# Optimization experiments

Hardware: AMD Instinct MI355X
Metric: run time of the kernel (lower is better)

## Reference

```python
import jax, jax.numpy as jnp
import numpy as np

T_STEPS = 128
N_RAYS = 16384
RAY_EXT = 10.0  # ray_ext_factor


def _posenc(x, n_freq=4):
    # x: (...,3) in [-1,1] -> (...,3 + 3*2*n_freq) = (...,27)
    feats = [x]
    for k in range(n_freq):
        f = (2.0 ** k) * jnp.pi
        feats.append(jnp.sin(f * x))
        feats.append(jnp.cos(f * x))
    return jnp.concatenate(feats, -1)


def _sh_deg2(d):
    # real spherical harmonics, degree 0 and 1 (4 coeffs), d unit vectors (...,3)
    x, y, z = d[..., 0], d[..., 1], d[..., 2]
    c0 = 0.28209479177387814
    c1 = 0.4886025119029199
    return jnp.stack([jnp.full_like(x, c0), c1 * y, c1 * z, c1 * x], -1)


def _forward(rays_o, rays_d, tnoise, aabb, W1, b1, W2, b2, Wc1, bc1, Wc2, bc2):
    # --- ray-AABB intersection (slab method), RayBundle.intersect_aabb ---
    inv_d = 1.0 / rays_d
    t0 = (aabb[0] - rays_o) * inv_d
    t1 = (aabb[1] - rays_o) * inv_d
    tnear = jnp.maximum(jnp.max(jnp.minimum(t0, t1), -1, keepdims=True), 0.0)  # (N,1)
    tfar = jnp.min(jnp.maximum(t0, t1), -1, keepdims=True)                      # (N,1)
    active = (tfar > tnear).astype(rays_o.dtype)  # active_mask; masking replaces compaction

    # --- StratifiedRayStepSampler: ts (T,N,1) ---
    T = tnoise.shape[0]
    base = (jnp.arange(T, dtype=rays_o.dtype)[:, None, None] + tnoise) / T
    ts = tnear[None] + (tfar - tnear)[None] * base
    xyz = rays_o[None] + ts * rays_d[None]  # (T,N,3)

    # --- vol.sample(xyz, ynm, return_color=True): density + color MLP ---
    xn = 2.0 * (xyz - aabb[0]) / (aabb[1] - aabb[0]) - 1.0
    enc = _posenc(xn)                             # (T,N,27)
    h = jax.nn.relu(enc @ W1 + b1)                # (T,N,64)
    dh = h @ W2 + b2                              # (T,N,16)
    sigma = jnp.exp(dh[..., :1])                  # (T,N,1) density
    feat = dh[..., 1:]                            # (T,N,15)
    dnorm = jnp.linalg.norm(rays_d, axis=-1, keepdims=True)  # (N,1)
    ynm = _sh_deg2(rays_d / dnorm)                # encode_raydir -> (N,4)
    ynm = jnp.broadcast_to(ynm[None], (T,) + ynm.shape)      # expand to (T,N,4)
    hc = jax.nn.relu(jnp.concatenate([feat, ynm], -1) @ Wc1 + bc1)
    rgb = jax.nn.sigmoid(hc @ Wc2 + bc2)          # (T,N,3)

    # --- integrate_timesteps: transmittance-weighted compositing ---
    tfinal = tfar * RAY_EXT
    delta = jnp.concatenate([ts[1:] - ts[:-1], tfinal[None] - ts[-1:]], 0)  # (T,N,1)
    sd = sigma * delta * dnorm[None]
    alpha = 1.0 - jnp.exp(-sd)
    trans = jnp.exp(-(jnp.cumsum(sd, 0) - sd))    # exclusive cumsum transmittance
    w = trans * alpha * active[None]              # (T,N,1); inactive rays -> zero maps

    color = jnp.sum(w * rgb, 0)                   # color_map  (N,3)
    alpha_map = jnp.sum(w, 0)                     # alpha_map  (N,1)
    return jnp.concatenate([color, alpha_map], -1)  # rgba (N,4)


def setup_inputs() -> dict:
    key = jax.random.key(0)
    ks = jax.random.split(key, 8)
    # origins on a sphere of radius 2.5 around the unit aabb, aimed at points inside it
    o = jax.random.normal(ks[0], (N_RAYS, 3), jnp.float32)
    o = 2.5 * o / jnp.linalg.norm(o, axis=-1, keepdims=True)
    tgt = jax.random.uniform(ks[1], (N_RAYS, 3), jnp.float32, -0.5, 0.5)
    d = tgt - o
    d = d / jnp.linalg.norm(d, axis=-1, keepdims=True)
    aabb = jnp.array([[-1.0, -1.0, -1.0], [1.0, 1.0, 1.0]], jnp.float32)
    tnoise = jax.random.uniform(ks[2], (T_STEPS, N_RAYS, 1), jnp.float32)
    s1, s2, s3, s4 = 27 ** -0.5, 64 ** -0.5, 19 ** -0.5, 64 ** -0.5
    return {
        'rays_o': o, 'rays_d': d, 'tnoise': tnoise, 'aabb': aabb,
        'W1': jax.random.normal(ks[3], (27, 64), jnp.float32) * s1,
        'b1': jnp.zeros((64,), jnp.float32),
        'W2': jax.random.normal(ks[4], (64, 16), jnp.float32) * (0.1 * s2),
        'b2': jnp.zeros((16,), jnp.float32),
        'Wc1': jax.random.normal(ks[5], (19, 64), jnp.float32) * s3,
        'bc1': jnp.zeros((64,), jnp.float32),
        'Wc2': jax.random.normal(ks[6], (64, 3), jnp.float32) * s4,
        'bc2': jnp.zeros((3,), jnp.float32),
    }


def reference(rays_o, rays_d, tnoise, aabb, W1, b1, W2, b2, Wc1, bc1, Wc2, bc2):
    return _forward(rays_o, rays_d, tnoise, aabb, W1, b1, W2, b2, Wc1, bc1, Wc2, bc2)
```

## Files before the change

kernel.cpp:

```cpp
#include <hip/hip_runtime.h>
#include <stdint.h>

#define N_RAYS  16384
#define T_STEPS 128
#define RPW   16
#define WAVES 4
#define TSEG  32

typedef _Float16 half8  __attribute__((ext_vector_type(8)));
typedef _Float16 half4  __attribute__((ext_vector_type(4)));
typedef __fp16   fp16x2 __attribute__((ext_vector_type(2)));
typedef float    float4_ __attribute__((ext_vector_type(4)));
typedef uint32_t uint2_  __attribute__((ext_vector_type(2)));

#define H8_W1    0
#define H8_W2    256
#define H8_WC2   384
#define H_WC1K16 4096
#define F32_CV   3072
#define F32_BC2  3392
#define F32_S0   3408

__device__ __forceinline__ uint32_t pk(float a, float b) {
    fp16x2 h = __builtin_amdgcn_cvt_pkrtz(a, b);
    return __builtin_bit_cast(uint32_t, h);
}
__device__ __forceinline__ uint32_t pkr(float a, float b) {
    fp16x2 h = __builtin_amdgcn_cvt_pkrtz(a, b);
    fp16x2 z = {(__fp16)0.f, (__fp16)0.f};
    fp16x2 m = __builtin_elementwise_max(h, z);
    return __builtin_bit_cast(uint32_t, m);
}

__global__ void prep_weights(const float* __restrict__ W1, const float* __restrict__ b1,
                             const float* __restrict__ W2, const float* __restrict__ b2,
                             const float* __restrict__ Wc1, const float* __restrict__ bc1,
                             const float* __restrict__ Wc2, const float* __restrict__ bc2,
                             void* __restrict__ ws) {
    _Float16* wh = (_Float16*)ws;
    float*    wf = (float*)ws;
    int frag = blockIdx.x;
    int lane = threadIdx.x;
    int mm = lane & 15, q = lane >> 4;
    if (frag < 4) {
        int tau = frag;
        int n = tau * 16 + mm;
        for (int j = 0; j < 8; ++j) {
            float w;
            if (j < 6)      w = W1[(3 + 6 * q + j) * 64 + n];
            else if (j == 6) w = (q == 0) ? W1[0 * 64 + n] : (q == 1) ? W1[2 * 64 + n] : 0.f;
            else             w = (q == 0) ? W1[1 * 64 + n] : (q == 1) ? b1[n] : 0.f;
            wh[(H8_W1 + tau * 64 + lane) * 8 + j] = (_Float16)w;
        }
    } else if (frag < 6) {
        int kap = frag - 4;
        for (int j = 0; j < 8; ++j) {
            int k = kap * 32 + q * 8 + j;
            wh[(H8_W2 + kap * 64 + lane) * 8 + j] = (_Float16)W2[k * 16 + mm];
        }
    } else if (frag < 10) {
        int tau = frag - 6;
        int n2 = tau * 16 + mm;
        for (int j = 0; j < 4; ++j) {
            int k = 4 * q + j;
            float w = (k == 0) ? 0.f : Wc1[(k - 1) * 64 + n2];
            wh[H_WC1K16 + (tau * 64 + lane) * 4 + j] = (_Float16)w;
        }
    } else if (frag < 12) {
        int kap = frag - 10;
        for (int j = 0; j < 8; ++j) {
            int k = kap * 32 + q * 8 + j;
            wh[(H8_WC2 + kap * 64 + lane) * 8 + j] =
                (_Float16)((mm < 3) ? Wc2[k * 3 + mm] : 0.f);
        }
    } else {
        int n = lane;
        wf[F32_CV + 0 * 64 + n] = Wc1[15 * 64 + n];
        wf[F32_CV + 1 * 64 + n] = Wc1[16 * 64 + n];
        wf[F32_CV + 2 * 64 + n] = Wc1[17 * 64 + n];
        wf[F32_CV + 3 * 64 + n] = Wc1[18 * 64 + n];
        float cc = bc1[n];
        for (int c = 0; c < 15; ++c) cc += b2[1 + c] * Wc1[c * 64 + n];
        wf[F32_CV + 4 * 64 + n] = cc;
        if (lane < 16) wf[F32_BC2 + lane] = (lane < 3) ? bc2[lane] : 0.f;
        if (lane == 0) wf[F32_S0] = b2[0];
    }
}

__global__ __launch_bounds__(256, 4)
void render_kernel(const float* __restrict__ rays_o, const float* __restrict__ rays_d,
                   const float* __restrict__ tnoise, const float* __restrict__ aabb,
                   const void* __restrict__ ws, float* __restrict__ out) {
    __shared__ __align__(16) _Float16 sH[WAVES][2][1024];
    __shared__ float sComb[WAVES][RPW][5];

    const int tid  = threadIdx.x;
    const int wv   = tid >> 6;
    const int lane = tid & 63;
    const int m    = lane & 15;
    const int q    = lane >> 4;
    const int r    = blockIdx.x * RPW + m;

    const half8* wsv  = (const half8*)ws;
    const half4* wsv4 = (const half4*)((const _Float16*)ws + H_WC1K16);
    const float* wsf  = (const float*)ws;
    half8 fW1[4], fW2[2], fWc2[2];
    half4 fWc1[4];
    #pragma unroll
    for (int i = 0; i < 4; ++i) fW1[i]  = wsv[H8_W1  + i * 64 + lane];
    #pragma unroll
    for (int i = 0; i < 2; ++i) fW2[i]  = wsv[H8_W2  + i * 64 + lane];
    #pragma unroll
    for (int i = 0; i < 2; ++i) fWc2[i] = wsv[H8_WC2 + i * 64 + lane];
    #pragma unroll
    for (int i = 0; i < 4; ++i) fWc1[i] = wsv4[i * 64 + lane];
    const float4_ binit = ((const float4_*)(wsf + F32_BC2))[q];
    const float s0b = wsf[F32_S0];

    float o0 = rays_o[r * 3 + 0], o1 = rays_o[r * 3 + 1], o2 = rays_o[r * 3 + 2];
    float d0 = rays_d[r * 3 + 0], d1 = rays_d[r * 3 + 1], d2 = rays_d[r * 3 + 2];
    float a00 = aabb[0], a01 = aabb[1], a02 = aabb[2];
    float a10 = aabb[3], a11 = aabb[4], a12 = aabb[5];

    float i0 = 1.0f / d0, i1 = 1.0f / d1, i2 = 1.0f / d2;
    float u0 = (a00 - o0) * i0, v0 = (a10 - o0) * i0;
    float u1 = (a01 - o1) * i1, v1 = (a11 - o1) * i1;
    float u2 = (a02 - o2) * i2, v2 = (a12 - o2) * i2;
    float tnear = fmaxf(fmaxf(fmaxf(fminf(u0, v0), fminf(u1, v1)), fminf(u2, v2)), 0.0f);
    float tfar  = fminf(fminf(fmaxf(u0, v0), fmaxf(u1, v1)), fmaxf(u2, v2));
    bool active = (tfar > tnear);
    float dt = tfar - tnear;
    float dt128 = dt * (1.0f / 128.0f);

    float dn  = sqrtf(d0 * d0 + d1 * d1 + d2 * d2);
    float idn = 1.0f / dn;
    const float c0sh = 0.28209479177387814f;
    const float c1sh = 0.4886025119029199f;
    float y1 = c1sh * d1 * idn, y2 = c1sh * d2 * idn, y3 = c1sh * d0 * idn;

    float4_ cv[4];
    #pragma unroll
    for (int tau = 0; tau < 4; ++tau) {
        #pragma unroll
        for (int reg = 0; reg < 4; ++reg) {
            int n = tau * 16 + 4 * q + reg;
            float c = wsf[F32_CV + 4 * 64 + n];
            c = fmaf(c0sh, wsf[F32_CV + 0 * 64 + n], c);
            c = fmaf(y1,   wsf[F32_CV + 1 * 64 + n], c);
            c = fmaf(y2,   wsf[F32_CV + 2 * 64 + n], c);
            c = fmaf(y3,   wsf[F32_CV + 3 * 64 + n], c);
            cv[tau][reg] = c;
        }
    }

    float qs = 0.5f * (float)(1 << q);
    float sc0 = 2.0f / (a10 - a00), of0 = -a00 * sc0 - 1.0f;
    float sc1 = 2.0f / (a11 - a01), of1 = -a01 * sc1 - 1.0f;
    float sc2 = 2.0f / (a12 - a02), of2 = -a02 * sc2 - 1.0f;
    float scq0 = sc0 * qs, ofq0 = of0 * qs;
    float scq1 = sc1 * qs, ofq1 = of1 * qs;
    float scq2 = sc2 * qs, ofq2 = of2 * qs;

    _Float16*       hwp[2];
    const _Float16* hrp[2];
    #pragma unroll
    for (int p = 0; p < 2; ++p) {
        hwp[p] = &sH[wv][p][((q >> 1) * 16 + m) * 8 + 4 * (q & 1)];
        hrp[p] = &sH[wv][p][(q * 16 + m) * 8];
    }

    const float4_ z4 = {0.f, 0.f, 0.f, 0.f};
    const bool q0 = (q == 0), q1 = (q == 1);

    float trans = 1.0f, sdtot = 0.0f, wacc = 0.0f;
    float cacc0 = 0.0f, cacc1 = 0.0f, cacc2 = 0.0f;

    const int tbase = wv * TSEG;
    float nA = tnoise[(tbase + 0) * N_RAYS + r];
    float nB = tnoise[(tbase + 1) * N_RAYS + r];

    #pragma unroll 1
    for (int tt = 0; tt < TSEG; tt += 2) {
        const int t0 = tbase + tt, t1 = t0 + 1;
        float nC = (t0 + 2 < T_STEPS) ? tnoise[(t0 + 2) * N_RAYS + r] : 0.0f;
        float nD = (t0 + 3 < T_STEPS) ? tnoise[(t0 + 3) * N_RAYS + r] : 0.0f;
        float ts0 = fmaf((float)t0 + nA, dt128, tnear);
        float ts1 = fmaf((float)t1 + nB, dt128, tnear);
        float ts2 = fmaf((float)(t0 + 2) + nC, dt128, tnear);
        float tsP[2] = {ts0, ts1};
        float deltaP[2];
        deltaP[0] = ts1 - ts0;
        deltaP[1] = (t1 < T_STEPS - 1) ? (ts2 - ts1) : fmaf(tfar, 10.0f, -ts1);
        nA = nC; nB = nD;

        float dhx[2];
        float4_ rgbP[2];

        #pragma unroll
        for (int p = 0; p < 2; ++p) {
            float x = fmaf(tsP[p], d0, o0);
            float y = fmaf(tsP[p], d1, o1);
            float z = fmaf(tsP[p], d2, o2);
            float xr0 = fmaf(x, scq0, ofq0);
            float xr1 = fmaf(y, scq1, ofq1);
            float xr2 = fmaf(z, scq2, ofq2);
            float s0 = __builtin_amdgcn_sinf(xr0);
            float s1 = __builtin_amdgcn_sinf(xr1);
            float s2 = __builtin_amdgcn_sinf(xr2);
            float cA = __builtin_amdgcn_cosf(xr0);
            float cB = __builtin_amdgcn_cosf(xr1);
            float cC = __builtin_amdgcn_cosf(xr2);
            float e6 = q0 ? (xr0 + xr0) : (q1 ? xr2 : 0.0f);
            float e7 = q0 ? (xr1 + xr1) : (q1 ? 1.0f : 0.0f);
            union { uint32_t u[4]; half8 h; } xf_;
            xf_.u[0] = pk(s0, s1); xf_.u[1] = pk(s2, cA);
            xf_.u[2] = pk(cB, cC); xf_.u[3] = pk(e6, e7);
            half8 xf = xf_.h;

            float4_ h0 = __builtin_amdgcn_mfma_f32_16x16x32_f16(fW1[0], xf, z4, 0, 0, 0);
            float4_ h1 = __builtin_amdgcn_mfma_f32_16x16x32_f16(fW1[1], xf, z4, 0, 0, 0);
            float4_ h2 = __builtin_amdgcn_mfma_f32_16x16x32_f16(fW1[2], xf, z4, 0, 0, 0);
            float4_ h3 = __builtin_amdgcn_mfma_f32_16x16x32_f16(fW1[3], xf, z4, 0, 0, 0);
            uint2_ w;
            w.x = pkr(h0.x, h0.y); w.y = pkr(h0.z, h0.w); *(uint2_*)(hwp[p] + 0 * 256) = w;
            w.x = pkr(h1.x, h1.y); w.y = pkr(h1.z, h1.w); *(uint2_*)(hwp[p] + 1 * 256) = w;
            w.x = pkr(h2.x, h2.y); w.y = pkr(h2.z, h2.w); *(uint2_*)(hwp[p] + 2 * 256) = w;
            w.x = pkr(h3.x, h3.y); w.y = pkr(h3.z, h3.w); *(uint2_*)(hwp[p] + 3 * 256) = w;
        }

        #pragma unroll
        for (int p = 0; p < 2; ++p) {
            half8 hb0 = *(const half8*)(hrp[p] + 0);
            half8 hb1 = *(const half8*)(hrp[p] + 512);
            float4_ dh = __builtin_amdgcn_mfma_f32_16x16x32_f16(fW2[0], hb0, z4, 0, 0, 0);
            dh = __builtin_amdgcn_mfma_f32_16x16x32_f16(fW2[1], hb1, dh, 0, 0, 0);
            dhx[p] = dh.x;

            union { uint32_t u[2]; half4 h; } bf_;
            bf_.u[0] = pk(dh.x, dh.y); bf_.u[1] = pk(dh.z, dh.w);
            half4 fb = bf_.h;

            float4_ t0v = __builtin_amdgcn_mfma_f32_16x16x16f16(fWc1[0], fb, cv[0], 0, 0, 0);
            float4_ t1v = __builtin_amdgcn_mfma_f32_16x16x16f16(fWc1[1], fb, cv[1], 0, 0, 0);
            float4_ t2v = __builtin_amdgcn_mfma_f32_16x16x16f16(fWc1[2], fb, cv[2], 0, 0, 0);
            float4_ t3v = __builtin_amdgcn_mfma_f32_16x16x16f16(fWc1[3], fb, cv[3], 0, 0, 0);
            uint2_ w;
            w.x = pkr(t0v.x, t0v.y); w.y = pkr(t0v.z, t0v.w); *(uint2_*)(hwp[p] + 0 * 256) = w;
            w.x = pkr(t1v.x, t1v.y); w.y = pkr(t1v.z, t1v.w); *(uint2_*)(hwp[p] + 1 * 256) = w;
            w.x = pkr(t2v.x, t2v.y); w.y = pkr(t2v.z, t2v.w); *(uint2_*)(hwp[p] + 2 * 256) = w;
            w.x = pkr(t3v.x, t3v.y); w.y = pkr(t3v.z, t3v.w); *(uint2_*)(hwp[p] + 3 * 256) = w;
        }

        #pragma unroll
        for (int p = 0; p < 2; ++p) {
            half8 cb0 = *(const half8*)(hrp[p] + 0);
            half8 cb1 = *(const half8*)(hrp[p] + 512);
            float4_ rgbp = __builtin_amdgcn_mfma_f32_16x16x32_f16(fWc2[0], cb0, binit, 0, 0, 0);
            rgbP[p] = __builtin_amdgcn_mfma_f32_16x16x32_f16(fWc2[1], cb1, rgbp, 0, 0, 0);
        }

        if (q == 0) {
            #pragma unroll
            for (int p = 0; p < 2; ++p) {
                float sigma = __expf(dhx[p] + s0b);
                float sd = sigma * deltaP[p] * dn;
                float e = __expf(-sd);
                float alpha = 1.0f - e;
                float w = trans * alpha;
                float rr = __builtin_amdgcn_rcpf(1.0f + __expf(-rgbP[p].x));
                float rg = __builtin_amdgcn_rcpf(1.0f + __expf(-rgbP[p].y));
                float rb = __builtin_amdgcn_rcpf(1.0f + __expf(-rgbP[p].z));
                cacc0 = fmaf(w, rr, cacc0);
                cacc1 = fmaf(w, rg, cacc1);
                cacc2 = fmaf(w, rb, cacc2);
                wacc += w;
                trans *= e;
                sdtot += sd;
            }
        }
    }

    if (q == 0) {
        sComb[wv][m][0] = sdtot;
        sComb[wv][m][1] = wacc;
        sComb[wv][m][2] = cacc0;
        sComb[wv][m][3] = cacc1;
        sComb[wv][m][4] = cacc2;
    }
    __syncthreads();

    if (tid < RPW) {
        float P = 1.0f, C0 = 0.0f, C1 = 0.0f, C2 = 0.0f, WS = 0.0f;
        #pragma unroll
        for (int s = 0; s < WAVES; ++s) {
            C0 = fmaf(P, sComb[s][tid][2], C0);
            C1 = fmaf(P, sComb[s][tid][3], C1);
            C2 = fmaf(P, sComb[s][tid][4], C2);
            WS = fmaf(P, sComb[s][tid][1], WS);
            P *= __expf(-sComb[s][tid][0]);
        }
        float act = active ? 1.0f : 0.0f;
        const int rg = blockIdx.x * RPW + tid;
        out[rg * 4 + 0] = C0 * act;
        out[rg * 4 + 1] = C1 * act;
        out[rg * 4 + 2] = C2 * act;
        out[rg * 4 + 3] = WS * act;
    }
}

extern "C" void kernel_launch(void* const* d_in, const int* in_sizes, int n_in,
                              void* d_out, int out_size, void* d_ws, size_t ws_size,
                              hipStream_t stream) {
    const float* rays_o = (const float*)d_in[0];
    const float* rays_d = (const float*)d_in[1];
    const float* tnoise = (const float*)d_in[2];
    const float* aabb   = (const float*)d_in[3];
    const float* W1  = (const float*)d_in[4];
    const float* b1  = (const float*)d_in[5];
    const float* W2  = (const float*)d_in[6];
    const float* b2  = (const float*)d_in[7];
    const float* Wc1 = (const float*)d_in[8];
    const float* bc1 = (const float*)d_in[9];
    const float* Wc2 = (const float*)d_in[10];
    const float* bc2 = (const float*)d_in[11];

    prep_weights<<<dim3(13), dim3(64), 0, stream>>>(W1, b1, W2, b2, Wc1, bc1, Wc2, bc2, d_ws);

    dim3 grid(N_RAYS / RPW);
    dim3 block(WAVES * 64);
    render_kernel<<<grid, block, 0, stream>>>(rays_o, rays_d, tnoise, aabb, d_ws,
                                              (float*)d_out);
}
```

Baseline: 120.9 us.

## Chain MLP layers in registers using 16x16x16 MFMAs instead of LDS round-trips

Removes the shared-memory staging buffer that transposed hidden activations between MLP layers. The output accumulator layout of each 16x16x16 MFMA is fed straight in as the B operand of the next layer, so the K=64 reductions become four chained 16x16x16 MFMAs instead of two 16x16x32 ones, with weights repacked into matching K16 fragments. This drops the LDS writes, reads and implied waits per step at the cost of more, smaller MFMA instructions and serial accumulator dependencies.

After: 122.4 us. Within noise of the previous version (+1.2%).

```diff
diff --git a/kernel.cpp b/kernel.cpp
--- a/kernel.cpp
+++ b/kernel.cpp
@@ -11,15 +11,13 @@
 typedef _Float16 half4  __attribute__((ext_vector_type(4)));
 typedef __fp16   fp16x2 __attribute__((ext_vector_type(2)));
 typedef float    float4_ __attribute__((ext_vector_type(4)));
-typedef uint32_t uint2_  __attribute__((ext_vector_type(2)));
-
-#define H8_W1    0
-#define H8_W2    256
-#define H8_WC2   384
-#define H_WC1K16 4096
-#define F32_CV   3072
-#define F32_BC2  3392
-#define F32_S0   3408
+
+#define H_W2K   2048
+#define H_WC1K  3072
+#define H_WC2K  4096
+#define F32_CV  2560
+#define F32_BC2 2880
+#define F32_S0  2896
 
 __device__ __forceinline__ uint32_t pk(float a, float b) {
     fp16x2 h = __builtin_amdgcn_cvt_pkrtz(a, b);
@@ -30,6 +28,11 @@
     fp16x2 z = {(__fp16)0.f, (__fp16)0.f};
     fp16x2 m = __builtin_elementwise_max(h, z);
     return __builtin_bit_cast(uint32_t, m);
+}
+__device__ __forceinline__ half4 mk4(uint32_t lo, uint32_t hi) {
+    union { uint32_t u[2]; half4 h; } v;
+    v.u[0] = lo; v.u[1] = hi;
+    return v.h;
 }
 
 __global__ void prep_weights(const float* __restrict__ W1, const float* __restrict__ b1,
@@ -50,27 +53,27 @@
             if (j < 6)      w = W1[(3 + 6 * q + j) * 64 + n];
             else if (j == 6) w = (q == 0) ? W1[0 * 64 + n] : (q == 1) ? W1[2 * 64 + n] : 0.f;
             else             w = (q == 0) ? W1[1 * 64 + n] : (q == 1) ? b1[n] : 0.f;
-            wh[(H8_W1 + tau * 64 + lane) * 8 + j] = (_Float16)w;
-        }
-    } else if (frag < 6) {
-        int kap = frag - 4;
-        for (int j = 0; j < 8; ++j) {
-            int k = kap * 32 + q * 8 + j;
-            wh[(H8_W2 + kap * 64 + lane) * 8 + j] = (_Float16)W2[k * 16 + mm];
-        }
-    } else if (frag < 10) {
-        int tau = frag - 6;
+            wh[(tau * 64 + lane) * 8 + j] = (_Float16)w;
+        }
+    } else if (frag < 8) {
+        int tau = frag - 4;
+        for (int j = 0; j < 4; ++j) {
+            int k = 16 * tau + 4 * q + j;
+            wh[H_W2K + (tau * 64 + lane) * 4 + j] = (_Float16)W2[k * 16 + mm];
+        }
+    } else if (frag < 12) {
+        int tau = frag - 8;
         int n2 = tau * 16 + mm;
         for (int j = 0; j < 4; ++j) {
             int k = 4 * q + j;
             float w = (k == 0) ? 0.f : Wc1[(k - 1) * 64 + n2];
-            wh[H_WC1K16 + (tau * 64 + lane) * 4 + j] = (_Float16)w;
-        }
-    } else if (frag < 12) {
-        int kap = frag - 10;
-        for (int j = 0; j < 8; ++j) {
-            int k = kap * 32 + q * 8 + j;
-            wh[(H8_WC2 + kap * 64 + lane) * 8 + j] =
+            wh[H_WC1K + (tau * 64 + lane) * 4 + j] = (_Float16)w;
+        }
+    } else if (frag < 16) {
+        int tau = frag - 12;
+        for (int j = 0; j < 4; ++j) {
+            int k = 16 * tau + 4 * q + j;
+            wh[H_WC2K + (tau * 64 + lane) * 4 + j] =
                 (_Float16)((mm < 3) ? Wc2[k * 3 + mm] : 0.f);
         }
     } else {
@@ -91,7 +94,6 @@
 void render_kernel(const float* __restrict__ rays_o, const float* __restrict__ rays_d,
                    const float* __restrict__ tnoise, const float* __restrict__ aabb,
                    const void* __restrict__ ws, float* __restrict__ out) {
-    __shared__ __align__(16) _Float16 sH[WAVES][2][1024];
     __shared__ float sComb[WAVES][RPW][5];
 
     const int tid  = threadIdx.x;
@@ -101,19 +103,21 @@
     const int q    = lane >> 4;
     const int r    = blockIdx.x * RPW + m;
 
-    const half8* wsv  = (const half8*)ws;
-    const half4* wsv4 = (const half4*)((const _Float16*)ws + H_WC1K16);
-    const float* wsf  = (const float*)ws;
-    half8 fW1[4], fW2[2], fWc2[2];
-    half4 fWc1[4];
-    #pragma unroll
-    for (int i = 0; i < 4; ++i) fW1[i]  = wsv[H8_W1  + i * 64 + lane];
-    #pragma unroll
-    for (int i = 0; i < 2; ++i) fW2[i]  = wsv[H8_W2  + i * 64 + lane];
-    #pragma unroll
-    for (int i = 0; i < 2; ++i) fWc2[i] = wsv[H8_WC2 + i * 64 + lane];
-    #pragma unroll
-    for (int i = 0; i < 4; ++i) fWc1[i] = wsv4[i * 64 + lane];
+    const half8* wsv   = (const half8*)ws;
+    const half4* w2k   = (const half4*)((const _Float16*)ws + H_W2K);
+    const half4* wc1k  = (const half4*)((const _Float16*)ws + H_WC1K);
+    const half4* wc2k  = (const half4*)((const _Float16*)ws + H_WC2K);
+    const float* wsf   = (const float*)ws;
+    half8 fW1[4];
+    half4 fW2[4], fWc1[4], fWc2[4];
+    #pragma unroll
+    for (int i = 0; i < 4; ++i) fW1[i]  = wsv[i * 64 + lane];
+    #pragma unroll
+    for (int i = 0; i < 4; ++i) fW2[i]  = w2k[i * 64 + lane];
+    #pragma unroll
+    for (int i = 0; i < 4; ++i) fWc1[i] = wc1k[i * 64 + lane];
+    #pragma unroll
+    for (int i = 0; i < 4; ++i) fWc2[i] = wc2k[i * 64 + lane];
     const float4_ binit = ((const float4_*)(wsf + F32_BC2))[q];
     const float s0b = wsf[F32_S0];
 
@@ -160,14 +164,6 @@
     float scq0 = sc0 * qs, ofq0 = of0 * qs;
     float scq1 = sc1 * qs, ofq1 = of1 * qs;
     float scq2 = sc2 * qs, ofq2 = of2 * qs;
-
-    _Float16*       hwp[2];
-    const _Float16* hrp[2];
-    #pragma unroll
-    for (int p = 0; p < 2; ++p) {
-        hwp[p] = &sH[wv][p][((q >> 1) * 16 + m) * 8 + 4 * (q & 1)];
-        hrp[p] = &sH[wv][p][(q * 16 + m) * 8];
-    }
 
     const float4_ z4 = {0.f, 0.f, 0.f, 0.f};
     const bool q0 = (q == 0), q1 = (q == 1);
@@ -221,42 +217,35 @@
             float4_ h1 = __builtin_amdgcn_mfma_f32_16x16x32_f16(fW1[1], xf, z4, 0, 0, 0);
             float4_ h2 = __builtin_amdgcn_mfma_f32_16x16x32_f16(fW1[2], xf, z4, 0, 0, 0);
             float4_ h3 = __builtin_amdgcn_mfma_f32_16x16x32_f16(fW1[3], xf, z4, 0, 0, 0);
-            uint2_ w;
-            w.x = pkr(h0.x, h0.y); w.y = pkr(h0.z, h0.w); *(uint2_*)(hwp[p] + 0 * 256) = w;
-            w.x = pkr(h1.x, h1.y); w.y = pkr(h1.z, h1.w); *(uint2_*)(hwp[p] + 1 * 256) = w;
-            w.x = pkr(h2.x, h2.y); w.y = pkr(h2.z, h2.w); *(uint2_*)(hwp[p] + 2 * 256) = w;
-            w.x = pkr(h3.x, h3.y); w.y = pkr(h3.z, h3.w); *(uint2_*)(hwp[p] + 3 * 256) = w;
-        }
-
-        #pragma unroll
-        for (int p = 0; p < 2; ++p) {
-            half8 hb0 = *(const half8*)(hrp[p] + 0);
-            half8 hb1 = *(const half8*)(hrp[p] + 512);
-            float4_ dh = __builtin_amdgcn_mfma_f32_16x16x32_f16(fW2[0], hb0, z4, 0, 0, 0);
-            dh = __builtin_amdgcn_mfma_f32_16x16x32_f16(fW2[1], hb1, dh, 0, 0, 0);
+
+            half4 hB0 = mk4(pkr(h0.x, h0.y), pkr(h0.z, h0.w));
+            half4 hB1 = mk4(pkr(h1.x, h1.y), pkr(h1.z, h1.w));
+            half4 hB2 = mk4(pkr(h2.x, h2.y), pkr(h2.z, h2.w));
+            half4 hB3 = mk4(pkr(h3.x, h3.y), pkr(h3.z, h3.w));
+
+            float4_ dh = __builtin_amdgcn_mfma_f32_16x16x16f16(fW2[0], hB0, z4, 0, 0, 0);
+            dh = __builtin_amdgcn_mfma_f32_16x16x16f16(fW2[1], hB1, dh, 0, 0, 0);
+            dh = __builtin_amdgcn_mfma_f32_16x16x16f16(fW2[2], hB2, dh, 0, 0, 0);
+            dh = __builtin_amdgcn_mfma_f32_16x16x16f16(fW2[3], hB3, dh, 0, 0, 0);
             dhx[p] = dh.x;
 
-            union { uint32_t u[2]; half4 h; } bf_;
-            bf_.u[0] = pk(dh.x, dh.y); bf_.u[1] = pk(dh.z, dh.w);
-            half4 fb = bf_.h;
+            half4 fb = mk4(pk(dh.x, dh.y), pk(dh.z, dh.w));
 
             float4_ t0v = __builtin_amdgcn_mfma_f32_16x16x16f16(fWc1[0], fb, cv[0], 0, 0, 0);
             float4_ t1v = __builtin_amdgcn_mfma_f32_16x16x16f16(fWc1[1], fb, cv[1], 0, 0, 0);
             float4_ t2v = __builtin_amdgcn_mfma_f32_16x16x16f16(fWc1[2], fb, cv[2], 0, 0, 0);
             float4_ t3v = __builtin_amdgcn_mfma_f32_16x16x16f16(fWc1[3], fb, cv[3], 0, 0, 0);
-            uint2_ w;
-            w.x = pkr(t0v.x, t0v.y); w.y = pkr(t0v.z, t0v.w); *(uint2_*)(hwp[p] + 0 * 256) = w;
-            w.x = pkr(t1v.x, t1v.y); w.y = pkr(t1v.z, t1v.w); *(uint2_*)(hwp[p] + 1 * 256) = w;
-            w.x = pkr(t2v.x, t2v.y); w.y = pkr(t2v.z, t2v.w); *(uint2_*)(hwp[p] + 2 * 256) = w;
-            w.x = pkr(t3v.x, t3v.y); w.y = pkr(t3v.z, t3v.w); *(uint2_*)(hwp[p] + 3 * 256) = w;
-        }
-
-        #pragma unroll
-        for (int p = 0; p < 2; ++p) {
-            half8 cb0 = *(const half8*)(hrp[p] + 0);
-            half8 cb1 = *(const half8*)(hrp[p] + 512);
-            float4_ rgbp = __builtin_amdgcn_mfma_f32_16x16x32_f16(fWc2[0], cb0, binit, 0, 0, 0);
-            rgbP[p] = __builtin_amdgcn_mfma_f32_16x16x32_f16(fWc2[1], cb1, rgbp, 0, 0, 0);
+
+            half4 cB0 = mk4(pkr(t0v.x, t0v.y), pkr(t0v.z, t0v.w));
+            half4 cB1 = mk4(pkr(t1v.x, t1v.y), pkr(t1v.z, t1v.w));
+            half4 cB2 = mk4(pkr(t2v.x, t2v.y), pkr(t2v.z, t2v.w));
+            half4 cB3 = mk4(pkr(t3v.x, t3v.y), pkr(t3v.z, t3v.w));
+
+            float4_ rgb = __builtin_amdgcn_mfma_f32_16x16x16f16(fWc2[0], cB0, binit, 0, 0, 0);
+            rgb = __builtin_amdgcn_mfma_f32_16x16x16f16(fWc2[1], cB1, rgb, 0, 0, 0);
+            rgb = __builtin_amdgcn_mfma_f32_16x16x16f16(fWc2[2], cB2, rgb, 0, 0, 0);
+            rgb = __builtin_amdgcn_mfma_f32_16x16x16f16(fWc2[3], cB3, rgb, 0, 0, 0);
+            rgbP[p] = rgb;
         }
 
         if (q == 0) {
@@ -324,7 +313,7 @@
     const float* Wc2 = (const float*)d_in[10];
     const float* bc2 = (const float*)d_in[11];
 
-    prep_weights<<<dim3(13), dim3(64), 0, stream>>>(W1, b1, W2, b2, Wc1, bc1, Wc2, bc2, d_ws);
+    prep_weights<<<dim3(17), dim3(64), 0, stream>>>(W1, b1, W2, b2, Wc1, bc1, Wc2, bc2, d_ws);
 
     dim3 grid(N_RAYS / RPW);
     dim3 block(WAVES * 64);
```
